# Optimization experiments

Measured on AMD Instinct MI355X. Metric: run time of the kernel, lower is better.

The kernel has to match this reference:

```python
import jax, jax.numpy as jnp
import numpy as np


def setup_inputs() -> dict:
    key = jax.random.key(0)
    ks = jax.random.split(key, 8)
    B, N, H = 8, 64, 256
    nE, E = 256, 64
    HID, OUT = 512, 1
    s1 = 1.0 / np.sqrt(H + E)
    s2 = 1.0 / np.sqrt(HID)
    return {
        "h_all": jax.random.normal(ks[0], (B, N, H), dtype=jnp.float32),
        "e_feat": jax.random.normal(ks[1], (nE, E), dtype=jnp.float32),
        "W1": jax.random.normal(ks[2], (H + E, HID), dtype=jnp.float32) * s1,
        "b1": jnp.zeros((HID,), dtype=jnp.float32),
        "W2": jax.random.normal(ks[3], (HID, HID), dtype=jnp.float32) * s2,
        "b2": jnp.zeros((HID,), dtype=jnp.float32),
        "W3": jax.random.normal(ks[4], (HID, OUT), dtype=jnp.float32) * s2,
        "b3": jnp.zeros((OUT,), dtype=jnp.float32),
    }


def reference(h_all, e_feat, W1, b1, W2, b2, W3, b3):
    # Math == MLP(cat([expand(h), expand(e)], -1)) but computed via split
    # weights: cat([h,e]) @ W1 == h @ W1[:H] + e @ W1[H:], avoiding the
    # materialized [B,N,nE,H+E] concat tensor.
    H = h_all.shape[-1]
    Wh, We = W1[:H], W1[H:]
    h_part = jnp.einsum("bnh,hk->bnk", h_all, Wh)        # [B,N,HID]
    e_part = jnp.einsum("ed,dk->ek", e_feat, We)          # [nE,HID]
    x = h_part[:, :, None, :] + e_part[None, None, :, :] + b1  # [B,N,nE,HID]
    x = jax.nn.relu(x)
    x = jax.nn.relu(jnp.einsum("bnek,kj->bnej", x, W2) + b2)
    return jnp.einsum("bnek,ko->bneo", x, W3) + b3        # [B,N,nE,OUT]
```

## Files before the change

### kernel.cpp

```cpp
#include <hip/hip_runtime.h>
#include <hip/hip_bf16.h>


typedef __attribute__((ext_vector_type(8))) short bf16x8;
typedef __attribute__((ext_vector_type(16))) float f32x16;

static __device__ __forceinline__ ushort2 pk_bf16(float a, float b) {
  union { __hip_bfloat162 h; ushort2 u; } c;
  c.h = __float22bfloat162_rn(make_float2(a, b));
  return c.u;
}
static __device__ __forceinline__ float bf2f(unsigned short u) {
  union { unsigned int i; float f; } c;
  c.i = ((unsigned int)u) << 16;
  return c.f;
}

__global__ __launch_bounds__(256) void k_prep(
    const float* __restrict__ h_all, const float* __restrict__ e_feat,
    const float* __restrict__ W1, const float* __restrict__ b1,
    const float* __restrict__ W2,
    unsigned short* __restrict__ hpb, unsigned short* __restrict__ epb,
    unsigned short* __restrict__ w2f) {
  __shared__ float sm[64 * 68];
  const int t = threadIdx.x;
  const int b = blockIdx.x;

  if (b < 256) {
    const int r0 = b * 2;
    float (*hs)[256] = (float(*)[256])sm;
    hs[0][t] = h_all[(size_t)r0 * 256 + t];
    hs[1][t] = h_all[(size_t)(r0 + 1) * 256 + t];
    __syncthreads();
    float2 a0 = make_float2(0.f, 0.f), a1 = make_float2(0.f, 0.f);
    #pragma unroll 2
    for (int k = 0; k < 256; k += 4) {
      float2 w0 = *(const float2*)(W1 + (size_t)k * 512 + 2 * t);
      float2 w1 = *(const float2*)(W1 + (size_t)(k + 1) * 512 + 2 * t);
      float2 w2v = *(const float2*)(W1 + (size_t)(k + 2) * 512 + 2 * t);
      float2 w3v = *(const float2*)(W1 + (size_t)(k + 3) * 512 + 2 * t);
      float h00 = hs[0][k], h01 = hs[0][k + 1], h02 = hs[0][k + 2], h03 = hs[0][k + 3];
      float h10 = hs[1][k], h11 = hs[1][k + 1], h12 = hs[1][k + 2], h13 = hs[1][k + 3];
      a0.x = fmaf(h00, w0.x, a0.x); a0.y = fmaf(h00, w0.y, a0.y);
      a1.x = fmaf(h10, w0.x, a1.x); a1.y = fmaf(h10, w0.y, a1.y);
      a0.x = fmaf(h01, w1.x, a0.x); a0.y = fmaf(h01, w1.y, a0.y);
      a1.x = fmaf(h11, w1.x, a1.x); a1.y = fmaf(h11, w1.y, a1.y);
      a0.x = fmaf(h02, w2v.x, a0.x); a0.y = fmaf(h02, w2v.y, a0.y);
      a1.x = fmaf(h12, w2v.x, a1.x); a1.y = fmaf(h12, w2v.y, a1.y);
      a0.x = fmaf(h03, w3v.x, a0.x); a0.y = fmaf(h03, w3v.y, a0.y);
      a1.x = fmaf(h13, w3v.x, a1.x); a1.y = fmaf(h13, w3v.y, a1.y);
    }
    float2 bv = *(const float2*)(b1 + 2 * t);
    *(ushort2*)(hpb + (size_t)r0 * 512 + 2 * t) = pk_bf16(a0.x + bv.x, a0.y + bv.y);
    *(ushort2*)(hpb + (size_t)(r0 + 1) * 512 + 2 * t) = pk_bf16(a1.x + bv.x, a1.y + bv.y);
  } else if (b < 288) {
    const int r0 = (b - 256) * 8;
    sm[t] = e_feat[(size_t)r0 * 64 + t];
    sm[256 + t] = e_feat[(size_t)r0 * 64 + 256 + t];
    __syncthreads();
    float2 acc[8];
    #pragma unroll
    for (int i = 0; i < 8; ++i) acc[i] = make_float2(0.f, 0.f);
    for (int k = 0; k < 64; ++k) {
      float2 wv = *(const float2*)(W1 + (size_t)(256 + k) * 512 + 2 * t);
      #pragma unroll
      for (int i = 0; i < 8; ++i) {
        acc[i].x = fmaf(sm[i * 64 + k], wv.x, acc[i].x);
        acc[i].y = fmaf(sm[i * 64 + k], wv.y, acc[i].y);
      }
    }
    #pragma unroll
    for (int i = 0; i < 8; ++i)
      *(ushort2*)(epb + (size_t)(r0 + i) * 512 + 2 * t) = pk_bf16(acc[i].x, acc[i].y);
  } else {
    const int bb2 = b - 288;
    const int k0 = (bb2 >> 3) * 64;
    const int c0 = (bb2 & 7) * 64;
    #pragma unroll
    for (int rr = 0; rr < 4; ++rr) {
      const int row = rr * 16 + (t >> 4);
      float4 v = *(const float4*)(W2 + (size_t)(k0 + row) * 512 + c0 + (t & 15) * 4);
      *(float4*)(&sm[row * 68 + (t & 15) * 4]) = v;
    }
    __syncthreads();
    #pragma unroll
    for (int s2 = 0; s2 < 2; ++s2) {
      const int s = t * 2 + s2;
      const int rec = s >> 6, l = s & 63;
      const int jg = (c0 >> 5) + (rec & 1);
      const int ks = (k0 >> 4) + (rec >> 1);
      const int cl = (rec & 1) * 32 + (l & 31);
      const int kl = (rec >> 1) * 16 + (l >> 5) * 8;
      union { ushort2 o[4]; uint4 v; } u;
      #pragma unroll
      for (int uu = 0; uu < 4; ++uu)
        u.o[uu] = pk_bf16(sm[(kl + 2 * uu) * 68 + cl], sm[(kl + 2 * uu + 1) * 68 + cl]);
      *(uint4*)(w2f + ((size_t)(jg * 32 + ks) * 64 + l) * 8) = u.v;
    }
  }
}

__global__ __launch_bounds__(512, 4) void k_main(
    const unsigned short* __restrict__ hpb, const unsigned short* __restrict__ epb,
    const unsigned short* __restrict__ w2f, const float* __restrict__ b2,
    const float* __restrict__ W3, const float* __restrict__ b3,
    float* __restrict__ out) {
  __shared__ unsigned short x1s[64 * 512];
  __shared__ float osum[8][64];

  const int t = threadIdx.x;
  const int lane = t & 63;
  const int w = t >> 6;
  const int l31 = lane & 31;
  const int half = lane >> 5;
  const int bn = blockIdx.x >> 2;
  const int e0 = (blockIdx.x & 3) << 6;

  const unsigned short* wrec0 = w2f + ((size_t)(w * 2 + 0) * 32 * 64 + lane) * 8;
  const unsigned short* wrec1 = w2f + ((size_t)(w * 2 + 1) * 32 * 64 + lane) * 8;
  bf16x8 bb[2][2];
  bb[0][0] = *(const bf16x8*)(wrec0);
  bb[0][1] = *(const bf16x8*)(wrec1);
  bb[1][0] = *(const bf16x8*)(wrec0 + 512);
  bb[1][1] = *(const bf16x8*)(wrec1 + 512);

  {
    const int r = t >> 3;
    const int c8 = t & 7;
    const unsigned short* hrow = hpb + (size_t)bn * 512 + c8 * 8;
    const unsigned short* erow = epb + (size_t)(e0 + r) * 512 + c8 * 8;
    const int slot = (r & 31) + ((c8 & 1) << 5);
    const int rec0 = (r >> 5) * 32 + (c8 >> 1);
    #pragma unroll
    for (int i = 0; i < 8; ++i) {
      union { uint4 v; unsigned short s[8]; } hv, ev, ov;
      hv.v = *(const uint4*)(hrow + i * 64);
      ev.v = *(const uint4*)(erow + i * 64);
      #pragma unroll
      for (int u = 0; u < 4; ++u) {
        ushort2 p = pk_bf16(fmaxf(bf2f(ev.s[2 * u]) + bf2f(hv.s[2 * u]), 0.f),
                            fmaxf(bf2f(ev.s[2 * u + 1]) + bf2f(hv.s[2 * u + 1]), 0.f));
        ov.s[2 * u] = p.x;
        ov.s[2 * u + 1] = p.y;
      }
      *(uint4*)(&x1s[((rec0 + i * 4) * 64 + slot) * 8]) = ov.v;
    }
  }
  __syncthreads();

  f32x16 acc[2][2] = {};
  const unsigned short* abase = x1s + (size_t)lane * 8;
  #pragma unroll 8
  for (int ks = 0; ks < 32; ++ks) {
    const int cur = ks & 1;
    const int kn = (ks + 2) & 31;
    bf16x8 a0 = *(const bf16x8*)(abase + (size_t)(0 * 32 + ks) * 512);
    bf16x8 a1 = *(const bf16x8*)(abase + (size_t)(1 * 32 + ks) * 512);
    acc[0][0] = __builtin_amdgcn_mfma_f32_32x32x16_bf16(a0, bb[cur][0], acc[0][0], 0, 0, 0);
    acc[0][1] = __builtin_amdgcn_mfma_f32_32x32x16_bf16(a0, bb[cur][1], acc[0][1], 0, 0, 0);
    acc[1][0] = __builtin_amdgcn_mfma_f32_32x32x16_bf16(a1, bb[cur][0], acc[1][0], 0, 0, 0);
    acc[1][1] = __builtin_amdgcn_mfma_f32_32x32x16_bf16(a1, bb[cur][1], acc[1][1], 0, 0, 0);
    bb[cur][0] = *(const bf16x8*)(wrec0 + (size_t)kn * 512);
    bb[cur][1] = *(const bf16x8*)(wrec1 + (size_t)kn * 512);
  }

  float b2v[2], w3v[2];
  #pragma unroll
  for (int ct = 0; ct < 2; ++ct) {
    const int n = w * 64 + ct * 32 + l31;
    b2v[ct] = b2[n];
    w3v[ct] = W3[n];
  }
  #pragma unroll
  for (int rt = 0; rt < 2; ++rt) {
    float part[16];
    #pragma unroll
    for (int g = 0; g < 16; ++g) {
      part[g] = fmaf(fmaxf(acc[rt][0][g] + b2v[0], 0.f), w3v[0], 0.f);
      part[g] = fmaf(fmaxf(acc[rt][1][g] + b2v[1], 0.f), w3v[1], part[g]);
    }
    #pragma unroll
    for (int g = 0; g < 16; ++g) {
      float v = part[g];
      v += __shfl_xor(v, 1);
      v += __shfl_xor(v, 2);
      v += __shfl_xor(v, 4);
      v += __shfl_xor(v, 8);
      v += __shfl_xor(v, 16);
      part[g] = v;
    }
    if (l31 == 0) {
      #pragma unroll
      for (int g = 0; g < 16; ++g) {
        const int row = rt * 32 + (g & 3) + 8 * (g >> 2) + 4 * half;
        osum[w][row] = part[g];
      }
    }
  }
  __syncthreads();
  if (t < 64) {
    float s = b3[0];
    #pragma unroll
    for (int ww = 0; ww < 8; ++ww) s += osum[ww][t];
    out[(size_t)bn * 256 + e0 + t] = s;
  }
}

extern "C" void kernel_launch(void* const* d_in, const int* in_sizes, int n_in,
                              void* d_out, int out_size, void* d_ws, size_t ws_size,
                              hipStream_t stream) {
  const float* h_all  = (const float*)d_in[0];
  const float* e_feat = (const float*)d_in[1];
  const float* W1     = (const float*)d_in[2];
  const float* b1     = (const float*)d_in[3];
  const float* W2     = (const float*)d_in[4];
  const float* b2     = (const float*)d_in[5];
  const float* W3     = (const float*)d_in[6];
  const float* b3     = (const float*)d_in[7];
  float* out = (float*)d_out;

  unsigned short* hpb = (unsigned short*)d_ws;
  unsigned short* epb = hpb + 512 * 512;
  unsigned short* w2f = epb + 256 * 512;

  hipLaunchKernelGGL(k_prep, dim3(352), dim3(256), 0, stream,
                     h_all, e_feat, W1, b1, W2, hpb, epb, w2f);
  hipLaunchKernelGGL(k_main, dim3(2048), dim3(512), 0, stream,
                     hpb, epb, w2f, b2, W3, b3, out);
}
```

Before: 162.7 us.

## Pre-swizzle e_part into MFMA fragment layout and deepen W2 register prefetch

The prep kernel now writes e_part directly in the MFMA A-fragment record layout per 64-row quarter. This lets the main kernel load it with fully contiguous uint4 reads and store x1 to LDS contiguously instead of scattering it, which is meant to cut address math and uncoalesced global reads in the x1 build phase. All global loads are issued up front before the add/relu. The W2 B-operand prefetch ring grows from 2 to 4 k-steps to hide global latency in the MFMA loop, at the cost of more VGPRs under the 512x4 launch bound.

```diff
diff --git a/kernel.cpp b/kernel.cpp
--- a/kernel.cpp
+++ b/kernel.cpp
@@ -20,7 +20,7 @@
     const float* __restrict__ h_all, const float* __restrict__ e_feat,
     const float* __restrict__ W1, const float* __restrict__ b1,
     const float* __restrict__ W2,
-    unsigned short* __restrict__ hpb, unsigned short* __restrict__ epb,
+    unsigned short* __restrict__ hpb, unsigned short* __restrict__ epf,
     unsigned short* __restrict__ w2f) {
   __shared__ float sm[64 * 68];
   const int t = threadIdx.x;
@@ -69,9 +69,19 @@
         acc[i].y = fmaf(sm[i * 64 + k], wv.y, acc[i].y);
       }
     }
-    #pragma unroll
-    for (int i = 0; i < 8; ++i)
-      *(ushort2*)(epb + (size_t)(r0 + i) * 512 + 2 * t) = pk_bf16(acc[i].x, acc[i].y);
+    const int k = 2 * t;
+    const int ks = k >> 4;
+    const int kh = (k >> 3) & 1;
+    const int j = k & 7;
+    #pragma unroll
+    for (int i = 0; i < 8; ++i) {
+      const int e = r0 + i;
+      const int q = e >> 6, er = e & 63;
+      const int rec = (er >> 5) * 32 + ks;
+      const int s = (er & 31) + (kh << 5);
+      *(ushort2*)(epf + (size_t)q * 32768 + ((size_t)(rec * 64 + s)) * 8 + j) =
+          pk_bf16(acc[i].x, acc[i].y);
+    }
   } else {
     const int bb2 = b - 288;
     const int k0 = (bb2 >> 3) * 64;
@@ -101,7 +111,7 @@
 }
 
 __global__ __launch_bounds__(512, 4) void k_main(
-    const unsigned short* __restrict__ hpb, const unsigned short* __restrict__ epb,
+    const unsigned short* __restrict__ hpb, const unsigned short* __restrict__ epf,
     const unsigned short* __restrict__ w2f, const float* __restrict__ b2,
     const float* __restrict__ W3, const float* __restrict__ b3,
     float* __restrict__ out) {
@@ -114,36 +124,40 @@
   const int l31 = lane & 31;
   const int half = lane >> 5;
   const int bn = blockIdx.x >> 2;
-  const int e0 = (blockIdx.x & 3) << 6;
+  const int q = blockIdx.x & 3;
 
   const unsigned short* wrec0 = w2f + ((size_t)(w * 2 + 0) * 32 * 64 + lane) * 8;
   const unsigned short* wrec1 = w2f + ((size_t)(w * 2 + 1) * 32 * 64 + lane) * 8;
-  bf16x8 bb[2][2];
-  bb[0][0] = *(const bf16x8*)(wrec0);
-  bb[0][1] = *(const bf16x8*)(wrec1);
-  bb[1][0] = *(const bf16x8*)(wrec0 + 512);
-  bb[1][1] = *(const bf16x8*)(wrec1 + 512);
+  bf16x8 bb[4][2];
+  #pragma unroll
+  for (int d = 0; d < 4; ++d) {
+    bb[d][0] = *(const bf16x8*)(wrec0 + (size_t)d * 512);
+    bb[d][1] = *(const bf16x8*)(wrec1 + (size_t)d * 512);
+  }
 
   {
-    const int r = t >> 3;
-    const int c8 = t & 7;
-    const unsigned short* hrow = hpb + (size_t)bn * 512 + c8 * 8;
-    const unsigned short* erow = epb + (size_t)(e0 + r) * 512 + c8 * 8;
-    const int slot = (r & 31) + ((c8 & 1) << 5);
-    const int rec0 = (r >> 5) * 32 + (c8 >> 1);
-    #pragma unroll
-    for (int i = 0; i < 8; ++i) {
-      union { uint4 v; unsigned short s[8]; } hv, ev, ov;
-      hv.v = *(const uint4*)(hrow + i * 64);
-      ev.v = *(const uint4*)(erow + i * 64);
+    const unsigned short* eq = epf + (size_t)q * 32768;
+    const unsigned short* hrow = hpb + (size_t)bn * 512;
+    uint4 ev[8], hv[8];
+    #pragma unroll
+    for (int p = 0; p < 8; ++p) {
+      ev[p] = *(const uint4*)(eq + ((size_t)p * 512 + t) * 8);
+      const int c = (((p * 8 + w) & 31) << 1) + ((t >> 5) & 1);
+      hv[p] = *(const uint4*)(hrow + c * 8);
+    }
+    #pragma unroll
+    for (int p = 0; p < 8; ++p) {
+      union { uint4 v; unsigned short s[8]; } e8, h8, ov;
+      e8.v = ev[p];
+      h8.v = hv[p];
       #pragma unroll
       for (int u = 0; u < 4; ++u) {
-        ushort2 p = pk_bf16(fmaxf(bf2f(ev.s[2 * u]) + bf2f(hv.s[2 * u]), 0.f),
-                            fmaxf(bf2f(ev.s[2 * u + 1]) + bf2f(hv.s[2 * u + 1]), 0.f));
-        ov.s[2 * u] = p.x;
-        ov.s[2 * u + 1] = p.y;
+        ushort2 pk = pk_bf16(fmaxf(bf2f(e8.s[2 * u]) + bf2f(h8.s[2 * u]), 0.f),
+                             fmaxf(bf2f(e8.s[2 * u + 1]) + bf2f(h8.s[2 * u + 1]), 0.f));
+        ov.s[2 * u] = pk.x;
+        ov.s[2 * u + 1] = pk.y;
       }
-      *(uint4*)(&x1s[((rec0 + i * 4) * 64 + slot) * 8]) = ov.v;
+      *(uint4*)(&x1s[((size_t)p * 512 + t) * 8]) = ov.v;
     }
   }
   __syncthreads();
@@ -152,16 +166,16 @@
   const unsigned short* abase = x1s + (size_t)lane * 8;
   #pragma unroll 8
   for (int ks = 0; ks < 32; ++ks) {
-    const int cur = ks & 1;
-    const int kn = (ks + 2) & 31;
+    const int d = ks & 3;
+    const int kn = (ks + 4) & 31;
     bf16x8 a0 = *(const bf16x8*)(abase + (size_t)(0 * 32 + ks) * 512);
     bf16x8 a1 = *(const bf16x8*)(abase + (size_t)(1 * 32 + ks) * 512);
-    acc[0][0] = __builtin_amdgcn_mfma_f32_32x32x16_bf16(a0, bb[cur][0], acc[0][0], 0, 0, 0);
-    acc[0][1] = __builtin_amdgcn_mfma_f32_32x32x16_bf16(a0, bb[cur][1], acc[0][1], 0, 0, 0);
-    acc[1][0] = __builtin_amdgcn_mfma_f32_32x32x16_bf16(a1, bb[cur][0], acc[1][0], 0, 0, 0);
-    acc[1][1] = __builtin_amdgcn_mfma_f32_32x32x16_bf16(a1, bb[cur][1], acc[1][1], 0, 0, 0);
-    bb[cur][0] = *(const bf16x8*)(wrec0 + (size_t)kn * 512);
-    bb[cur][1] = *(const bf16x8*)(wrec1 + (size_t)kn * 512);
+    acc[0][0] = __builtin_amdgcn_mfma_f32_32x32x16_bf16(a0, bb[d][0], acc[0][0], 0, 0, 0);
+    acc[0][1] = __builtin_amdgcn_mfma_f32_32x32x16_bf16(a0, bb[d][1], acc[0][1], 0, 0, 0);
+    acc[1][0] = __builtin_amdgcn_mfma_f32_32x32x16_bf16(a1, bb[d][0], acc[1][0], 0, 0, 0);
+    acc[1][1] = __builtin_amdgcn_mfma_f32_32x32x16_bf16(a1, bb[d][1], acc[1][1], 0, 0, 0);
+    bb[d][0] = *(const bf16x8*)(wrec0 + (size_t)kn * 512);
+    bb[d][1] = *(const bf16x8*)(wrec1 + (size_t)kn * 512);
   }
 
   float b2v[2], w3v[2];
@@ -202,7 +216,7 @@
     float s = b3[0];
     #pragma unroll
     for (int ww = 0; ww < 8; ++ww) s += osum[ww][t];
-    out[(size_t)bn * 256 + e0 + t] = s;
+    out[(size_t)bn * 256 + (q << 6) + t] = s;
   }
 }
 
@@ -220,11 +234,11 @@
   float* out = (float*)d_out;
 
   unsigned short* hpb = (unsigned short*)d_ws;
-  unsigned short* epb = hpb + 512 * 512;
-  unsigned short* w2f = epb + 256 * 512;
+  unsigned short* epf = hpb + 512 * 512;
+  unsigned short* w2f = epf + 256 * 512;
 
   hipLaunchKernelGGL(k_prep, dim3(352), dim3(256), 0, stream,
-                     h_all, e_feat, W1, b1, W2, hpb, epb, w2f);
+                     h_all, e_feat, W1, b1, W2, hpb, epf, w2f);
   hipLaunchKernelGGL(k_main, dim3(2048), dim3(512), 0, stream,
-                     hpb, epb, w2f, b2, W3, b3, out);
-}
+                     hpb, epf, w2f, b2, W3, b3, out);
+}
```

Measured after the change: 159.8 us. About the same (-1.8%).
